# Kernel optimization log

Measured on AMD Instinct MI355X. Metric: run time of the kernel, lower is better.

## Reference

```python
import jax, jax.numpy as jnp
import numpy as np
import math

VOCAB = 50000; D = 512; DEPTH = 6; N = 16; DCONV = 4; R = 32; DFF = 4 * D
B = 2; L = 1024

# A = -exp(A_log) with A_log = log(arange(1..N)) repeated over D  =>  A[d,n] = -(n+1)
A_CONT = -jnp.broadcast_to(jnp.arange(1.0, N + 1, dtype=jnp.float32), (D, N))


def sinusoidal(t, dim):
    half = dim // 2
    f = jnp.exp(jnp.arange(half, dtype=jnp.float32) * (-math.log(10000.0) / (half - 1)))
    e = t.astype(jnp.float32)[:, None] * f[None, :]
    return jnp.concatenate([jnp.sin(e), jnp.cos(e)], axis=-1)


def layernorm(x, g, b, eps=1e-5):
    mu = jnp.mean(x, -1, keepdims=True)
    var = jnp.mean((x - mu) ** 2, -1, keepdims=True)
    return (x - mu) * jax.lax.rsqrt(var + eps) * g + b


def ssm(x, Win, Wconv, Wdt, bdt, Dp, Wout):
    # x: [B,L,D]
    proj = x @ Win.T  # [B,L,2D+R+2N]
    xc, z, dtu, Bp, Cp = jnp.split(proj, [D, 2 * D, 2 * D + R, 2 * D + R + N], axis=-1)
    # depthwise causal conv (left pad d_conv-1 == pad both + truncate to L)
    conv = jax.lax.conv_general_dilated(
        xc.transpose(0, 2, 1), Wconv, (1,), [(DCONV - 1, 0)],
        dimension_numbers=('NCH', 'OIH', 'NCH'), feature_group_count=D)
    u = jax.nn.silu(conv.transpose(0, 2, 1))  # [B,L,D]
    dt = jax.nn.softplus(dtu @ Wdt.T + bdt)   # [B,L,D]
    At = jnp.exp(dt[..., None] * A_CONT)      # [B,L,D,N] (ZOH)
    Bu = ((At - 1.0) / (A_CONT + 1e-10)) * Bp[:, :, None, :] * u[..., None]  # [B,L,D,N]

    def step(h, xs):
        a, bu, c = xs
        h = a * h + bu                       # [B,D,N]
        return h, jnp.einsum('bn,bdn->bd', c, h)

    h0 = jnp.zeros((x.shape[0], D, N), dtype=x.dtype)
    _, ys = jax.lax.scan(step, h0, (At.transpose(1, 0, 2, 3), Bu.transpose(1, 0, 2, 3), Cp.transpose(1, 0, 2)))
    y = ys.transpose(1, 0, 2)                # [B,L,D]
    y = (y + u * Dp) * jax.nn.silu(z)
    return y @ Wout.T


def setup_inputs():
    key = jax.random.key(0)
    ks = iter(jax.random.split(key, 32))
    nrm = lambda shape: jax.random.normal(next(ks), shape, jnp.float32) * 0.02
    inp = {
        'x_t': jax.random.randint(next(ks), (B, L), 0, VOCAB + 1),
        't': jax.random.randint(next(ks), (B,), 0, 100),
        'tok_emb': nrm((VOCAB + 1, D)),
        'tmlp_w1': nrm((4 * D, D)), 'tmlp_b1': jnp.zeros((4 * D,)),
        'tmlp_w2': nrm((D, 4 * D)), 'tmlp_b2': jnp.zeros((D,)),
        'ln1_g': jnp.ones((DEPTH, D)), 'ln1_b': jnp.zeros((DEPTH, D)),
        'in_w': nrm((DEPTH, 2 * D + R + 2 * N, D)),
        'conv_w': nrm((DEPTH, D, 1, DCONV)),
        'dt_w': nrm((DEPTH, D, R)), 'dt_b': jnp.zeros((DEPTH, D)),
        'D_p': jnp.ones((DEPTH, D)),
        'out_w': nrm((DEPTH, D, D)),
        'ln2_g': jnp.ones((DEPTH, D)), 'ln2_b': jnp.zeros((DEPTH, D)),
        'mlp_w1': nrm((DEPTH, DFF, D)), 'mlp_b1': jnp.zeros((DEPTH, DFF)),
        'mlp_w2': nrm((DEPTH, D, DFF)), 'mlp_b2': jnp.zeros((DEPTH, D)),
        'lno_g': jnp.ones((D,)), 'lno_b': jnp.zeros((D,)),
        'head_w': nrm((VOCAB, D)), 'head_b': jnp.zeros((VOCAB,)),
    }
    return inp


def reference(x_t, t, tok_emb, tmlp_w1, tmlp_b1, tmlp_w2, tmlp_b2,
              ln1_g, ln1_b, in_w, conv_w, dt_w, dt_b, D_p, out_w,
              ln2_g, ln2_b, mlp_w1, mlp_b1, mlp_w2, mlp_b2,
              lno_g, lno_b, head_w, head_b):
    te = sinusoidal(t, D)
    te = jax.nn.silu(te @ tmlp_w1.T + tmlp_b1) @ tmlp_w2.T + tmlp_b2  # [B,D]
    x = tok_emb[x_t] + te[:, None, :]                                  # [B,L,D]
    for i in range(DEPTH):
        x = x + ssm(layernorm(x, ln1_g[i], ln1_b[i]),
                    in_w[i], conv_w[i], dt_w[i], dt_b[i], D_p[i], out_w[i])
        h = layernorm(x, ln2_g[i], ln2_b[i])
        x = x + jax.nn.gelu(h @ mlp_w1[i].T + mlp_b1[i], approximate=False) @ mlp_w2[i].T + mlp_b2[i]
    x = layernorm(x, lno_g, lno_b)
    return x @ head_w.T + head_b  # [B,L,VOCAB]
```

## Files before the change

### kernel.cpp

```cpp
#include <hip/hip_runtime.h>
#include <hip/hip_bf16.h>
#include <math.h>

typedef __hip_bfloat16 bf16;
typedef short s16x8 __attribute__((ext_vector_type(8)));
typedef float f32x4 __attribute__((ext_vector_type(4)));

#define M_TOK 2048
#define DD    512
#define LSEQ  1024
#define PW    1088
#define NST   16
#define RR    32
#define DFFW  2048
#define NCH   64
#define CH    16
#define PAD   36
#define NHEAD 50000
#define NHEADP 50048

__device__ __forceinline__ float bf2f(bf16 v) { return __bfloat162float(v); }
__device__ __forceinline__ float siluf(float x) { return x / (1.f + expf(-x)); }

__device__ __forceinline__ s16x8 cvt8(const f32x4& a, const f32x4& b) {
  s16x8 r;
  r[0] = (short)__bfloat16_as_ushort(__float2bfloat16(a[0]));
  r[1] = (short)__bfloat16_as_ushort(__float2bfloat16(a[1]));
  r[2] = (short)__bfloat16_as_ushort(__float2bfloat16(a[2]));
  r[3] = (short)__bfloat16_as_ushort(__float2bfloat16(a[3]));
  r[4] = (short)__bfloat16_as_ushort(__float2bfloat16(b[0]));
  r[5] = (short)__bfloat16_as_ushort(__float2bfloat16(b[1]));
  r[6] = (short)__bfloat16_as_ushort(__float2bfloat16(b[2]));
  r[7] = (short)__bfloat16_as_ushort(__float2bfloat16(b[3]));
  return r;
}

__device__ __forceinline__ void gload16(const bf16* g, bf16* l) {
  __builtin_amdgcn_global_load_lds((const __attribute__((address_space(1))) void*)g,
                                   (__attribute__((address_space(3))) void*)l, 16, 0, 0);
}

__constant__ float c_invn[NST] = {
  -1.f/1, -1.f/2, -1.f/3, -1.f/4, -1.f/5, -1.f/6, -1.f/7, -1.f/8,
  -1.f/9, -1.f/10, -1.f/11, -1.f/12, -1.f/13, -1.f/14, -1.f/15, -1.f/16 };

__global__ __launch_bounds__(256) void k_cvt(
    const float* __restrict__ src, bf16* __restrict__ dst, int n_src, int n_dst)
{
  for (int i = (blockIdx.x * 256 + threadIdx.x) * 8; i < n_dst; i += gridDim.x * 256 * 8) {
    s16x8 v;
    if (i + 8 <= n_src) {
      f32x4 a = *(const f32x4*)(src + i), b = *(const f32x4*)(src + i + 4);
      v = cvt8(a, b);
    } else {
      v = (s16x8){0,0,0,0,0,0,0,0};
    }
    *(s16x8*)((short*)dst + i) = v;
  }
}

__global__ __launch_bounds__(256) void k_te1(
    const int* __restrict__ t, const float* __restrict__ w1, const float* __restrict__ b1,
    float* __restrict__ h1)
{
  __shared__ float semb[2][512];
  int tid = threadIdx.x;
  float t0 = (float)t[0], t1 = (float)t[1];
  {
    int k = tid;
    float f = expf((float)k * (-9.210340371976184f / 255.f));
    semb[0][k]       = sinf(t0 * f);
    semb[0][k + 256] = cosf(t0 * f);
    semb[1][k]       = sinf(t1 * f);
    semb[1][k + 256] = cosf(t1 * f);
  }
  __syncthreads();
  int wave = tid >> 6, lane = tid & 63;
  int j = blockIdx.x * 4 + wave;
  const float* wr = w1 + (size_t)j * 512;
  float s0 = 0.f, s1 = 0.f;
#pragma unroll
  for (int i = 0; i < 8; ++i) {
    int k = lane + (i << 6);
    float wv = wr[k];
    s0 += wv * semb[0][k];
    s1 += wv * semb[1][k];
  }
  for (int o = 32; o; o >>= 1) { s0 += __shfl_down(s0, o); s1 += __shfl_down(s1, o); }
  if (!lane) {
    float bv = b1[j];
    h1[j]        = siluf(s0 + bv);
    h1[2048 + j] = siluf(s1 + bv);
  }
}

__global__ __launch_bounds__(256) void k_te2(
    const float* __restrict__ h1, const float* __restrict__ w2, const float* __restrict__ b2,
    float* __restrict__ te)
{
  __shared__ float sh1[2][2048];
  int tid = threadIdx.x;
  for (int idx = tid; idx < 4096; idx += 256)
    sh1[idx >> 11][idx & 2047] = h1[idx];
  __syncthreads();
  int wave = tid >> 6, lane = tid & 63;
  int d = blockIdx.x * 4 + wave;
  const float* wr = w2 + (size_t)d * 2048;
  float s0 = 0.f, s1 = 0.f;
#pragma unroll
  for (int i = 0; i < 32; ++i) {
    int k = lane + (i << 6);
    float wv = wr[k];
    s0 += wv * sh1[0][k];
    s1 += wv * sh1[1][k];
  }
  for (int o = 32; o; o >>= 1) { s0 += __shfl_down(s0, o); s1 += __shfl_down(s1, o); }
  if (!lane) {
    float bv = b2[d];
    te[d]       = s0 + bv;
    te[512 + d] = s1 + bv;
  }
}

__global__ __launch_bounds__(256) void k_embed(
    const int* __restrict__ x_t, const float* __restrict__ tok,
    const float* __restrict__ te, float* __restrict__ x)
{
  int m = blockIdx.x;
  int b = m >> 10;
  int row = x_t[m];
  const float* src = tok + (size_t)row * DD;
  for (int d = threadIdx.x; d < DD; d += 256)
    x[(size_t)m * DD + d] = src[d] + te[b * DD + d];
}

__global__ __launch_bounds__(256) void k_layernorm(
    const float* __restrict__ x, const float* __restrict__ g, const float* __restrict__ bb,
    bf16* __restrict__ out)
{
  int m = blockIdx.x;
  const float* xr = x + (size_t)m * DD;
  float2 v = ((const float2*)xr)[threadIdx.x];
  float s = v.x + v.y, ss = v.x * v.x + v.y * v.y;
  for (int o = 32; o; o >>= 1) { s += __shfl_down(s, o); ss += __shfl_down(ss, o); }
  __shared__ float ps[4], pss[4];
  int wave = threadIdx.x >> 6, lane = threadIdx.x & 63;
  if (!lane) { ps[wave] = s; pss[wave] = ss; }
  __syncthreads();
  s = ps[0] + ps[1] + ps[2] + ps[3];
  ss = pss[0] + pss[1] + pss[2] + pss[3];
  float mu = s * (1.f / DD);
  float var = ss * (1.f / DD) - mu * mu;
  float inv = rsqrtf(var + 1e-5f);
  int d = threadIdx.x * 2;
  out[(size_t)m * DD + d]     = __float2bfloat16((v.x - mu) * inv * g[d]     + bb[d]);
  out[(size_t)m * DD + d + 1] = __float2bfloat16((v.y - mu) * inv * g[d + 1] + bb[d + 1]);
}

__global__ __launch_bounds__(128) void k_scan1f(
    const float* __restrict__ proj, const float* __restrict__ convw,
    const float* __restrict__ dtw, const float* __restrict__ dtb,
    float* __restrict__ ubuf, float* __restrict__ yloc,
    float* __restrict__ Ebuf, float* __restrict__ Aprod, float* __restrict__ hend)
{
  int d = (blockIdx.x << 7) + threadIdx.x;
  int c = blockIdx.y, b = blockIdx.z;
  int m0 = b * LSEQ + c * CH;
  __shared__ float sBC[CH][32];
  __shared__ float sDT[CH][32];
  for (int idx = threadIdx.x; idx < CH * 32; idx += 128) {
    int l = idx >> 5, j = idx & 31;
    sBC[l][j] = proj[(size_t)(m0 + l) * PW + 2 * DD + RR + j];
    sDT[l][j] = proj[(size_t)(m0 + l) * PW + 2 * DD + j];
  }
  __syncthreads();
  float cw0 = convw[d * 4], cw1 = convw[d * 4 + 1], cw2 = convw[d * 4 + 2], cw3 = convw[d * 4 + 3];
  float dtbd = dtb[d];
  f32x4 wr[8];
#pragma unroll
  for (int i = 0; i < 8; ++i) wr[i] = *(const f32x4*)(dtw + (size_t)d * RR + i * 4);
  float w0 = 0.f, w1 = 0.f, w2 = 0.f;
  {
    int l0 = c * CH;
    if (l0 >= 3) w0 = proj[(size_t)(m0 - 3) * PW + d];
    if (l0 >= 2) w1 = proj[(size_t)(m0 - 2) * PW + d];
    if (l0 >= 1) w2 = proj[(size_t)(m0 - 1) * PW + d];
  }
  float h[NST];
#pragma unroll
  for (int n = 0; n < NST; ++n) h[n] = 0.f;
  float S = 0.f;
  for (int l = 0; l < CH; ++l) {
    size_t m = (size_t)(m0 + l);
    float xc = proj[m * PW + d];
    float cv = w0 * cw0 + w1 * cw1 + w2 * cw2 + xc * cw3;
    w0 = w1; w1 = w2; w2 = xc;
    float uv = siluf(cv);
    ubuf[m * DD + d] = uv;
    float s = dtbd;
#pragma unroll
    for (int i = 0; i < 8; ++i) {
      f32x4 q = *(const f32x4*)&sDT[l][i * 4];
      s += q[0] * wr[i][0] + q[1] * wr[i][1] + q[2] * wr[i][2] + q[3] * wr[i][3];
    }
    float dtv = (s > 0.f) ? (s + log1pf(expf(-s))) : log1pf(expf(s));
    float e1 = expf(-dtv);
    S += dtv;
    Ebuf[m * DD + d] = expf(-S);
    float p = 1.f, acc = 0.f;
#pragma unroll
    for (int n = 0; n < NST; ++n) {
      p *= e1;
      float bu = (p - 1.f) * c_invn[n] * sBC[l][n] * uv;
      h[n] = p * h[n] + bu;
      acc += sBC[l][16 + n] * h[n];
    }
    yloc[m * DD + d] = acc;
  }
  float Ec = expf(-S);
  float p = 1.f;
  size_t base = ((size_t)(b * NCH + c) * NST) * DD + d;
#pragma unroll
  for (int n = 0; n < NST; ++n) {
    p *= Ec;
    Aprod[base + (size_t)n * DD] = p;
    hend [base + (size_t)n * DD] = h[n];
  }
}

__global__ __launch_bounds__(256) void k_scan2w(
    const float* __restrict__ Aprod, const float* __restrict__ hend, float* __restrict__ h0)
{
  int wave = threadIdx.x >> 6, lane = threadIdx.x & 63;
  int chain = blockIdx.x * 4 + wave;
  int d = chain & 511;
  int n = (chain >> 9) & 15;
  int b = chain >> 13;
  size_t o = ((size_t)((b * NCH + lane) * NST + n)) * DD + d;
  float A = Aprod[o], h = hend[o];
#pragma unroll
  for (int off = 1; off < 64; off <<= 1) {
    float Ap = __shfl_up(A, off);
    float hp = __shfl_up(h, off);
    if (lane >= off) { h = A * hp + h; A = A * Ap; }
  }
  float hprev = __shfl_up(h, 1);
  h0[o] = (lane == 0) ? 0.f : hprev;
}

__global__ __launch_bounds__(128) void k_scan3(
    const float* __restrict__ proj, const float* __restrict__ u,
    const float* __restrict__ yloc, const float* __restrict__ Ebuf,
    const float* __restrict__ h0, const float* __restrict__ Dp, bf16* __restrict__ out)
{
  int d = (blockIdx.x << 7) + threadIdx.x;
  int c = blockIdx.y, b = blockIdx.z;
  int m0 = b * LSEQ + c * CH;
  __shared__ float sC[CH][NST];
  for (int idx = threadIdx.x; idx < CH * NST; idx += 128)
    sC[idx >> 4][idx & 15] = proj[(size_t)(m0 + (idx >> 4)) * PW + 2 * DD + RR + NST + (idx & 15)];
  __syncthreads();
  float hh[NST];
  size_t base = ((size_t)(b * NCH + c) * NST) * DD + d;
#pragma unroll
  for (int n = 0; n < NST; ++n) hh[n] = h0[base + (size_t)n * DD];
  float dpv = Dp[d];
  for (int l = 0; l < CH; ++l) {
    size_t m = (size_t)(m0 + l);
    float E = Ebuf[m * DD + d];
    float p = 1.f, corr = 0.f;
#pragma unroll
    for (int n = 0; n < NST; ++n) {
      p *= E;
      corr += sC[l][n] * p * hh[n];
    }
    float y = yloc[m * DD + d] + corr;
    float z = proj[m * PW + DD + d];
    float v = (y + u[m * DD + d] * dpv) * siluf(z);
    out[m * DD + d] = __float2bfloat16(v);
  }
}

template<int ACT, bool BF16OUT, bool RES, bool BIAS>
__global__ __launch_bounds__(256) void gemm_bb64k(
    const bf16* __restrict__ A, const bf16* __restrict__ B,
    const float* __restrict__ bias, const float* __restrict__ res,
    void* __restrict__ Cout, int N, int K)
{
  __shared__ bf16 sA[2][64 * 32];
  __shared__ bf16 sB[2][64 * 32];
  int flat = blockIdx.y * gridDim.x + blockIdx.x;
  int qq = (gridDim.x * gridDim.y) >> 3;
  int s = (flat & 7) * qq + (flat >> 3);
  int bm = (s % gridDim.x) * 64;
  int bn = (s / gridDim.x) * 64;
  int tid = threadIdx.x;
  int wave = tid >> 6, lane = tid & 63;
  int wm = (wave >> 1) << 5, wn = (wave & 1) << 5;
  int r = lane & 15, q = lane >> 4;
  int srow = (wave << 4) + (lane >> 2);
  int scol = (lane & 3) << 3;
  const bf16* pA = A + (size_t)(bm + srow) * K + scol;
  const bf16* pB = B + (size_t)(bn + srow) * K + scol;
  int lofs = (wave << 4) << 5;

  f32x4 acc[2][2];
#pragma unroll
  for (int i = 0; i < 2; ++i)
#pragma unroll
    for (int j = 0; j < 2; ++j) acc[i][j] = (f32x4){0.f, 0.f, 0.f, 0.f};

  for (int k0 = 0; k0 < K; k0 += 64) {
    gload16(pA,      sA[0] + lofs);
    gload16(pA + 32, sA[1] + lofs);
    gload16(pB,      sB[0] + lofs);
    gload16(pB + 32, sB[1] + lofs);
    pA += 64; pB += 64;
    __syncthreads();
#pragma unroll
    for (int kk = 0; kk < 2; ++kk) {
      s16x8 af[2], bg[2];
#pragma unroll
      for (int i = 0; i < 2; ++i) af[i] = *(s16x8*)&sA[kk][((wm + i * 16 + r) << 5) + (q << 3)];
#pragma unroll
      for (int j = 0; j < 2; ++j) bg[j] = *(s16x8*)&sB[kk][((wn + j * 16 + r) << 5) + (q << 3)];
#pragma unroll
      for (int i = 0; i < 2; ++i)
#pragma unroll
        for (int j = 0; j < 2; ++j)
          acc[i][j] = __builtin_amdgcn_mfma_f32_16x16x32_bf16(af[i], bg[j], acc[i][j], 0, 0, 0);
    }
    __syncthreads();
  }

#pragma unroll
  for (int i = 0; i < 2; ++i)
#pragma unroll
    for (int j = 0; j < 2; ++j) {
      int n = bn + wn + j * 16 + r;
#pragma unroll
      for (int e = 0; e < 4; ++e) {
        int m = bm + wm + i * 16 + (q << 2) + e;
        float v = acc[i][j][e];
        if (BIAS) v += bias[n];
        if (ACT == 1) v = 0.5f * v * (1.f + erff(v * 0.70710678118f));
        if (RES) v += res[(size_t)m * N + n];
        if (BF16OUT) ((bf16*)Cout)[(size_t)m * N + n] = __float2bfloat16(v);
        else         ((float*)Cout)[(size_t)m * N + n] = v;
      }
    }
}

template<int ACT, bool BF16OUT, bool RES, bool BIAS>
__global__ __launch_bounds__(256) void gemm_bb128k(
    const bf16* __restrict__ A, const bf16* __restrict__ B,
    const float* __restrict__ bias, const float* __restrict__ res,
    void* __restrict__ Cout, int N, int K)
{
  __shared__ bf16 sA[2][128 * 32];
  __shared__ bf16 sB[2][128 * 32];
  int flat = blockIdx.y * gridDim.x + blockIdx.x;
  int qq = (gridDim.x * gridDim.y) >> 3;
  int s = (flat & 7) * qq + (flat >> 3);
  int bm = (s % gridDim.x) * 128;
  int bn = (s / gridDim.x) * 128;
  int tid = threadIdx.x;
  int wave = tid >> 6, lane = tid & 63;
  int wm = (wave >> 1) << 6, wn = (wave & 1) << 6;
  int r = lane & 15, q = lane >> 4;
  int srow = (wave << 4) + (lane >> 2);
  int scol = (lane & 3) << 3;
  const bf16* pA = A + (size_t)(bm + srow) * K + scol;
  const bf16* pB = B + (size_t)(bn + srow) * K + scol;
  int lofs = (wave << 4) << 5;

  f32x4 acc[4][4];
#pragma unroll
  for (int i = 0; i < 4; ++i)
#pragma unroll
    for (int j = 0; j < 4; ++j) acc[i][j] = (f32x4){0.f, 0.f, 0.f, 0.f};

  for (int k0 = 0; k0 < K; k0 += 64) {
    gload16(pA,                       sA[0] + lofs);
    gload16(pA + (size_t)64 * K,      sA[0] + lofs + 64 * 32);
    gload16(pA + 32,                  sA[1] + lofs);
    gload16(pA + (size_t)64 * K + 32, sA[1] + lofs + 64 * 32);
    gload16(pB,                       sB[0] + lofs);
    gload16(pB + (size_t)64 * K,      sB[0] + lofs + 64 * 32);
    gload16(pB + 32,                  sB[1] + lofs);
    gload16(pB + (size_t)64 * K + 32, sB[1] + lofs + 64 * 32);
    pA += 64; pB += 64;
    __syncthreads();
#pragma unroll
    for (int kk = 0; kk < 2; ++kk) {
      s16x8 af[4], bg[4];
#pragma unroll
      for (int i = 0; i < 4; ++i) af[i] = *(s16x8*)&sA[kk][((wm + i * 16 + r) << 5) + (q << 3)];
#pragma unroll
      for (int j = 0; j < 4; ++j) bg[j] = *(s16x8*)&sB[kk][((wn + j * 16 + r) << 5) + (q << 3)];
#pragma unroll
      for (int i = 0; i < 4; ++i)
#pragma unroll
        for (int j = 0; j < 4; ++j)
          acc[i][j] = __builtin_amdgcn_mfma_f32_16x16x32_bf16(af[i], bg[j], acc[i][j], 0, 0, 0);
    }
    __syncthreads();
  }

#pragma unroll
  for (int i = 0; i < 4; ++i)
#pragma unroll
    for (int j = 0; j < 4; ++j) {
      int n = bn + wn + j * 16 + r;
      if (n >= N) continue;
#pragma unroll
      for (int e = 0; e < 4; ++e) {
        int m = bm + wm + i * 16 + (q << 2) + e;
        float v = acc[i][j][e];
        if (BIAS) v += bias[n];
        if (ACT == 1) v = 0.5f * v * (1.f + erff(v * 0.70710678118f));
        if (RES) v += res[(size_t)m * N + n];
        if (BF16OUT) ((bf16*)Cout)[(size_t)m * N + n] = __float2bfloat16(v);
        else         ((float*)Cout)[(size_t)m * N + n] = v;
      }
    }
}

template<int ACT, bool BF16OUT, bool RES, bool BIAS, bool SWZ>
__global__ __launch_bounds__(256) void gemm_abt(
    const bf16* __restrict__ A, const float* __restrict__ B,
    const float* __restrict__ bias, const float* __restrict__ res,
    void* __restrict__ Cout, int N, int K)
{
  __shared__ bf16 sA[128][PAD];
  __shared__ bf16 sB[128][PAD];
  int bn, bm;
  if (SWZ) {
    int flat = blockIdx.y * gridDim.x + blockIdx.x;
    int q = (gridDim.x * gridDim.y) >> 3;
    int s = (flat & 7) * q + (flat >> 3);
    bm = (s % gridDim.x) * 128;
    bn = (s / gridDim.x) * 128;
  } else {
    bn = blockIdx.x * 128;
    bm = blockIdx.y * 128;
  }
  int tid = threadIdx.x;
  int wave = tid >> 6, lane = tid & 63;
  int wm = (wave >> 1) << 6, wn = (wave & 1) << 6;
  int r = lane & 15, q = lane >> 4;
  int ldr = tid >> 2;
  int ldc = (tid & 3) << 3;
  f32x4 acc[4][4];
#pragma unroll
  for (int i = 0; i < 4; ++i)
#pragma unroll
    for (int j = 0; j < 4; ++j) acc[i][j] = (f32x4){0.f, 0.f, 0.f, 0.f};
  s16x8 pa[2];
  f32x4 pb[2][2];
#define GLOAD(k0)                                                              \
  {                                                                            \
    _Pragma("unroll")                                                          \
    for (int h = 0; h < 2; ++h) {                                              \
      int row = ldr + (h << 6);                                                \
      pa[h] = *(const s16x8*)(A + (size_t)(bm + row) * K + (k0) + ldc);        \
      int nrow = bn + row;                                                     \
      if (nrow < N) {                                                          \
        const float* src = B + (size_t)nrow * K + (k0) + ldc;                  \
        pb[h][0] = *(const f32x4*)src;                                         \
        pb[h][1] = *(const f32x4*)(src + 4);                                   \
      } else {                                                                 \
        pb[h][0] = (f32x4){0.f,0.f,0.f,0.f};                                   \
        pb[h][1] = (f32x4){0.f,0.f,0.f,0.f};                                   \
      }                                                                        \
    }                                                                          \
  }
  GLOAD(0);
  for (int k0 = 0; k0 < K; k0 += 32) {
#pragma unroll
    for (int h = 0; h < 2; ++h) {
      int row = ldr + (h << 6);
      *(s16x8*)&sA[row][ldc] = pa[h];
      *(s16x8*)&sB[row][ldc] = cvt8(pb[h][0], pb[h][1]);
    }
    __syncthreads();
    if (k0 + 32 < K) GLOAD(k0 + 32);
    s16x8 af[4], bg[4];
#pragma unroll
    for (int i = 0; i < 4; ++i) af[i] = *(s16x8*)&sA[wm + i * 16 + r][q << 3];
#pragma unroll
    for (int j = 0; j < 4; ++j) bg[j] = *(s16x8*)&sB[wn + j * 16 + r][q << 3];
#pragma unroll
    for (int i = 0; i < 4; ++i)
#pragma unroll
      for (int j = 0; j < 4; ++j)
        acc[i][j] = __builtin_amdgcn_mfma_f32_16x16x32_bf16(af[i], bg[j], acc[i][j], 0, 0, 0);
    __syncthreads();
  }
#undef GLOAD
#pragma unroll
  for (int i = 0; i < 4; ++i)
#pragma unroll
    for (int j = 0; j < 4; ++j) {
      int n = bn + wn + j * 16 + r;
      if (n >= N) continue;
#pragma unroll
      for (int e = 0; e < 4; ++e) {
        int m = bm + wm + i * 16 + (q << 2) + e;
        float v = acc[i][j][e];
        if (BIAS) v += bias[n];
        if (ACT == 1) v = 0.5f * v * (1.f + erff(v * 0.70710678118f));
        if (RES) v += res[(size_t)m * N + n];
        if (BF16OUT) ((bf16*)Cout)[(size_t)m * N + n] = __float2bfloat16(v);
        else         ((float*)Cout)[(size_t)m * N + n] = v;
      }
    }
}

template<int ACT, bool BF16OUT, bool RES, bool BIAS>
__global__ __launch_bounds__(256) void gemm64(
    const bf16* __restrict__ A, const float* __restrict__ B,
    const float* __restrict__ bias, const float* __restrict__ res,
    void* __restrict__ Cout, int N, int K)
{
  __shared__ bf16 sA[64][PAD];
  __shared__ bf16 sB[64][PAD];
  int bn = blockIdx.x * 64;
  int bm = blockIdx.y * 64;
  int tid = threadIdx.x;
  int wave = tid >> 6, lane = tid & 63;
  int wm = (wave >> 1) << 5, wn = (wave & 1) << 5;
  int r = lane & 15, q = lane >> 4;
  int ldr = tid >> 2;
  int ldc = (tid & 3) << 3;
  f32x4 acc[2][2];
#pragma unroll
  for (int i = 0; i < 2; ++i)
#pragma unroll
    for (int j = 0; j < 2; ++j) acc[i][j] = (f32x4){0.f, 0.f, 0.f, 0.f};
  s16x8 pa;
  f32x4 pb[2];
#define GLOAD64(k0)                                                            \
  {                                                                            \
    pa = *(const s16x8*)(A + (size_t)(bm + ldr) * K + (k0) + ldc);             \
    const float* src = B + (size_t)(bn + ldr) * K + (k0) + ldc;                \
    pb[0] = *(const f32x4*)src;                                                \
    pb[1] = *(const f32x4*)(src + 4);                                          \
  }
  GLOAD64(0);
  for (int k0 = 0; k0 < K; k0 += 32) {
    *(s16x8*)&sA[ldr][ldc] = pa;
    *(s16x8*)&sB[ldr][ldc] = cvt8(pb[0], pb[1]);
    __syncthreads();
    if (k0 + 32 < K) GLOAD64(k0 + 32);
    s16x8 af[2], bg[2];
#pragma unroll
    for (int i = 0; i < 2; ++i) af[i] = *(s16x8*)&sA[wm + i * 16 + r][q << 3];
#pragma unroll
    for (int j = 0; j < 2; ++j) bg[j] = *(s16x8*)&sB[wn + j * 16 + r][q << 3];
#pragma unroll
    for (int i = 0; i < 2; ++i)
#pragma unroll
      for (int j = 0; j < 2; ++j)
        acc[i][j] = __builtin_amdgcn_mfma_f32_16x16x32_bf16(af[i], bg[j], acc[i][j], 0, 0, 0);
    __syncthreads();
  }
#undef GLOAD64
#pragma unroll
  for (int i = 0; i < 2; ++i)
#pragma unroll
    for (int j = 0; j < 2; ++j) {
      int n = bn + wn + j * 16 + r;
#pragma unroll
      for (int e = 0; e < 4; ++e) {
        int m = bm + wm + i * 16 + (q << 2) + e;
        float v = acc[i][j][e];
        if (BIAS) v += bias[n];
        if (ACT == 1) v = 0.5f * v * (1.f + erff(v * 0.70710678118f));
        if (RES) v += res[(size_t)m * N + n];
        if (BF16OUT) ((bf16*)Cout)[(size_t)m * N + n] = __float2bfloat16(v);
        else         ((float*)Cout)[(size_t)m * N + n] = v;
      }
    }
}

extern "C" void kernel_launch(void* const* d_in, const int* in_sizes, int n_in,
                              void* d_out, int out_size, void* d_ws, size_t ws_size,
                              hipStream_t stream) {
  const int*   x_t     = (const int*)d_in[0];
  const int*   t       = (const int*)d_in[1];
  const float* tok_emb = (const float*)d_in[2];
  const float* tmlp_w1 = (const float*)d_in[3];
  const float* tmlp_b1 = (const float*)d_in[4];
  const float* tmlp_w2 = (const float*)d_in[5];
  const float* tmlp_b2 = (const float*)d_in[6];
  const float* ln1_g   = (const float*)d_in[7];
  const float* ln1_b   = (const float*)d_in[8];
  const float* in_w    = (const float*)d_in[9];
  const float* conv_w  = (const float*)d_in[10];
  const float* dt_w    = (const float*)d_in[11];
  const float* dt_b    = (const float*)d_in[12];
  const float* D_p     = (const float*)d_in[13];
  const float* out_w   = (const float*)d_in[14];
  const float* ln2_g   = (const float*)d_in[15];
  const float* ln2_b   = (const float*)d_in[16];
  const float* mlp_w1  = (const float*)d_in[17];
  const float* mlp_b1  = (const float*)d_in[18];
  const float* mlp_w2  = (const float*)d_in[19];
  const float* mlp_b2  = (const float*)d_in[20];
  const float* lno_g   = (const float*)d_in[21];
  const float* lno_b   = (const float*)d_in[22];
  const float* head_w  = (const float*)d_in[23];
  const float* head_b  = (const float*)d_in[24];

  char* w = (char*)d_ws;
  float* te    = (float*)w;  w += 4096;
  float* h1t   = (float*)w;  w += 16384;
  float* x     = (float*)w;  w += (size_t)M_TOK * DD * 4;
  bf16*  aIn   = (bf16*)w;   w += (size_t)M_TOK * DD * 2;
  float* proj  = (float*)w;  w += (size_t)M_TOK * PW * 4;
  float* ubuf  = (float*)w;  w += (size_t)M_TOK * DD * 4;
  float* ybuf  = (float*)w;  w += (size_t)M_TOK * DD * 4;
  float* Ebuf  = (float*)w;  w += (size_t)M_TOK * DD * 4;
  float* Aprod = (float*)w;  w += (size_t)2 * NCH * NST * DD * 4;
  float* hend  = (float*)w;  w += (size_t)2 * NCH * NST * DD * 4;
  float* h0    = (float*)w;  w += (size_t)2 * NCH * NST * DD * 4;
  bf16*  gbuf  = (bf16*)proj;
  bf16* bw_in   = (bf16*)w;  w += (size_t)6 * PW * DD * 2;
  bf16* bw_out  = (bf16*)w;  w += (size_t)6 * DD * DD * 2;
  bf16* bw_m1   = (bf16*)w;  w += (size_t)6 * DFFW * DD * 2;
  bf16* bw_m2   = (bf16*)w;  w += (size_t)6 * DD * DFFW * 2;
  bf16* bw_head = (bf16*)w;  w += (size_t)NHEADP * DD * 2;
  bool fast = ((size_t)(w - (char*)d_ws) <= ws_size);

  if (fast) {
    k_cvt<<<1024, 256, 0, stream>>>(in_w,   bw_in,   6 * PW * DD,   6 * PW * DD);
    k_cvt<<<1024, 256, 0, stream>>>(out_w,  bw_out,  6 * DD * DD,   6 * DD * DD);
    k_cvt<<<1024, 256, 0, stream>>>(mlp_w1, bw_m1,   6 * DFFW * DD, 6 * DFFW * DD);
    k_cvt<<<1024, 256, 0, stream>>>(mlp_w2, bw_m2,   6 * DD * DFFW, 6 * DD * DFFW);
    k_cvt<<<2048, 256, 0, stream>>>(head_w, bw_head, NHEAD * DD,    NHEADP * DD);
  }

  k_te1<<<512, 256, 0, stream>>>(t, tmlp_w1, tmlp_b1, h1t);
  k_te2<<<128, 256, 0, stream>>>(h1t, tmlp_w2, tmlp_b2, te);
  k_embed<<<M_TOK, 256, 0, stream>>>(x_t, tok_emb, te, x);

  for (int i = 0; i < 6; ++i) {
    const float* cw_i   = conv_w + (size_t)i * DD * 4;
    const float* dtw_i  = dt_w   + (size_t)i * DD * RR;
    const float* dtb_i  = dt_b   + (size_t)i * DD;
    const float* dp_i   = D_p    + (size_t)i * DD;
    const float* m1b_i  = mlp_b1 + (size_t)i * DFFW;
    const float* m2b_i  = mlp_b2 + (size_t)i * DD;

    k_layernorm<<<M_TOK, 256, 0, stream>>>(x, ln1_g + i * DD, ln1_b + i * DD, aIn);
    if (fast)
      gemm_bb64k<0,false,false,false><<<dim3(M_TOK / 64, PW / 64), 256, 0, stream>>>(
          aIn, bw_in + (size_t)i * PW * DD, nullptr, nullptr, proj, PW, DD);
    else
      gemm64<0,false,false,false><<<dim3(PW / 64, M_TOK / 64), 256, 0, stream>>>(
          aIn, in_w + (size_t)i * PW * DD, nullptr, nullptr, proj, PW, DD);
    k_scan1f<<<dim3(4, NCH, 2), 128, 0, stream>>>(proj, cw_i, dtw_i, dtb_i,
                                                  ubuf, ybuf, Ebuf, Aprod, hend);
    k_scan2w<<<2 * NST * DD / 4, 256, 0, stream>>>(Aprod, hend, h0);
    k_scan3<<<dim3(4, NCH, 2), 128, 0, stream>>>(proj, ubuf, ybuf, Ebuf, h0, dp_i, aIn);
    if (fast) {
      gemm_bb64k<0,false,true,false><<<dim3(M_TOK / 64, DD / 64), 256, 0, stream>>>(
          aIn, bw_out + (size_t)i * DD * DD, nullptr, x, x, DD, DD);
      k_layernorm<<<M_TOK, 256, 0, stream>>>(x, ln2_g + i * DD, ln2_b + i * DD, aIn);
      gemm_bb64k<1,true,false,true><<<dim3(M_TOK / 64, DFFW / 64), 256, 0, stream>>>(
          aIn, bw_m1 + (size_t)i * DFFW * DD, m1b_i, nullptr, gbuf, DFFW, DD);
      gemm_bb64k<0,false,true,true><<<dim3(M_TOK / 64, DD / 64), 256, 0, stream>>>(
          gbuf, bw_m2 + (size_t)i * DD * DFFW, m2b_i, x, x, DD, DFFW);
    } else {
      gemm64<0,false,true,false><<<dim3(DD / 64, M_TOK / 64), 256, 0, stream>>>(
          aIn, out_w + (size_t)i * DD * DD, nullptr, x, x, DD, DD);
      k_layernorm<<<M_TOK, 256, 0, stream>>>(x, ln2_g + i * DD, ln2_b + i * DD, aIn);
      gemm64<1,true,false,true><<<dim3(DFFW / 64, M_TOK / 64), 256, 0, stream>>>(
          aIn, mlp_w1 + (size_t)i * DFFW * DD, m1b_i, nullptr, gbuf, DFFW, DD);
      gemm64<0,false,true,true><<<dim3(DD / 64, M_TOK / 64), 256, 0, stream>>>(
          gbuf, mlp_w2 + (size_t)i * DD * DFFW, m2b_i, x, x, DD, DFFW);
    }
  }

  k_layernorm<<<M_TOK, 256, 0, stream>>>(x, lno_g, lno_b, aIn);
  if (fast)
    gemm_bb128k<0,false,false,true><<<dim3(M_TOK / 128, NHEADP / 128), 256, 0, stream>>>(
        aIn, bw_head, head_b, nullptr, d_out, NHEAD, DD);
  else
    gemm_abt<0,false,false,true,true><<<dim3(M_TOK / 128, (NHEAD + 127) / 128), 256, 0, stream>>>(
        aIn, head_w, head_b, nullptr, d_out, NHEAD, DD);
}
```

Baseline: 1.086 ms.

## Use 256x256 double-buffered tile GEMM for vocab head projection

Replaces the 128x128 head GEMM with a dedicated 512-thread kernel using 256x256 output tiles, so each wave computes a 128x64 sub-tile. It also adds prefetch double-buffering over K=32 slices, loading the next slice while MFMAs run on the current one. The padded head width is raised to a multiple of 256 so the grid tiles evenly. The aim is more operand reuse per LDS byte and hiding global load latency, at the cost of higher register pressure (128 accumulator floats per thread) and more padded work at the vocab edge.

```diff
diff --git a/kernel.cpp b/kernel.cpp
--- a/kernel.cpp
+++ b/kernel.cpp
@@ -17,7 +17,7 @@
 #define CH    16
 #define PAD   36
 #define NHEAD 50000
-#define NHEADP 50048
+#define NHEADP 50176
 
 __device__ __forceinline__ float bf2f(bf16 v) { return __bfloat162float(v); }
 __device__ __forceinline__ float siluf(float x) { return x / (1.f + expf(-x)); }
@@ -351,22 +351,22 @@
     }
 }
 
-template<int ACT, bool BF16OUT, bool RES, bool BIAS>
-__global__ __launch_bounds__(256) void gemm_bb128k(
+template<bool BIAS>
+__global__ __launch_bounds__(512) void gemm_bhead256(
     const bf16* __restrict__ A, const bf16* __restrict__ B,
-    const float* __restrict__ bias, const float* __restrict__ res,
-    void* __restrict__ Cout, int N, int K)
-{
-  __shared__ bf16 sA[2][128 * 32];
-  __shared__ bf16 sB[2][128 * 32];
+    const float* __restrict__ bias, float* __restrict__ C, int N, int K)
+{
+  __shared__ bf16 sA[2][256 * 32];
+  __shared__ bf16 sB[2][256 * 32];
   int flat = blockIdx.y * gridDim.x + blockIdx.x;
   int qq = (gridDim.x * gridDim.y) >> 3;
   int s = (flat & 7) * qq + (flat >> 3);
-  int bm = (s % gridDim.x) * 128;
-  int bn = (s / gridDim.x) * 128;
+  int bm = (s % gridDim.x) * 256;
+  int bn = (s / gridDim.x) * 256;
   int tid = threadIdx.x;
   int wave = tid >> 6, lane = tid & 63;
-  int wm = (wave >> 1) << 6, wn = (wave & 1) << 6;
+  int wm = (wave >> 2) << 7;
+  int wn = (wave & 3) << 6;
   int r = lane & 15, q = lane >> 4;
   int srow = (wave << 4) + (lane >> 2);
   int scol = (lane & 3) << 3;
@@ -374,41 +374,44 @@
   const bf16* pB = B + (size_t)(bn + srow) * K + scol;
   int lofs = (wave << 4) << 5;
 
-  f32x4 acc[4][4];
-#pragma unroll
-  for (int i = 0; i < 4; ++i)
+  f32x4 acc[8][4];
+#pragma unroll
+  for (int i = 0; i < 8; ++i)
 #pragma unroll
     for (int j = 0; j < 4; ++j) acc[i][j] = (f32x4){0.f, 0.f, 0.f, 0.f};
 
-  for (int k0 = 0; k0 < K; k0 += 64) {
-    gload16(pA,                       sA[0] + lofs);
-    gload16(pA + (size_t)64 * K,      sA[0] + lofs + 64 * 32);
-    gload16(pA + 32,                  sA[1] + lofs);
-    gload16(pA + (size_t)64 * K + 32, sA[1] + lofs + 64 * 32);
-    gload16(pB,                       sB[0] + lofs);
-    gload16(pB + (size_t)64 * K,      sB[0] + lofs + 64 * 32);
-    gload16(pB + 32,                  sB[1] + lofs);
-    gload16(pB + (size_t)64 * K + 32, sB[1] + lofs + 64 * 32);
-    pA += 64; pB += 64;
+  gload16(pA,                   sA[0] + lofs);
+  gload16(pA + (size_t)128 * K, sA[0] + lofs + 128 * 32);
+  gload16(pB,                   sB[0] + lofs);
+  gload16(pB + (size_t)128 * K, sB[0] + lofs + 128 * 32);
+  pA += 32; pB += 32;
+  __syncthreads();
+
+  int cur = 0;
+  for (int k0 = 0; k0 < K; k0 += 32) {
+    if (k0 + 32 < K) {
+      gload16(pA,                   sA[cur ^ 1] + lofs);
+      gload16(pA + (size_t)128 * K, sA[cur ^ 1] + lofs + 128 * 32);
+      gload16(pB,                   sB[cur ^ 1] + lofs);
+      gload16(pB + (size_t)128 * K, sB[cur ^ 1] + lofs + 128 * 32);
+      pA += 32; pB += 32;
+    }
+    s16x8 bg[4];
+#pragma unroll
+    for (int j = 0; j < 4; ++j) bg[j] = *(s16x8*)&sB[cur][((wn + j * 16 + r) << 5) + (q << 3)];
+#pragma unroll
+    for (int i = 0; i < 8; ++i) {
+      s16x8 af = *(s16x8*)&sA[cur][((wm + i * 16 + r) << 5) + (q << 3)];
+#pragma unroll
+      for (int j = 0; j < 4; ++j)
+        acc[i][j] = __builtin_amdgcn_mfma_f32_16x16x32_bf16(af, bg[j], acc[i][j], 0, 0, 0);
+    }
     __syncthreads();
-#pragma unroll
-    for (int kk = 0; kk < 2; ++kk) {
-      s16x8 af[4], bg[4];
-#pragma unroll
-      for (int i = 0; i < 4; ++i) af[i] = *(s16x8*)&sA[kk][((wm + i * 16 + r) << 5) + (q << 3)];
-#pragma unroll
-      for (int j = 0; j < 4; ++j) bg[j] = *(s16x8*)&sB[kk][((wn + j * 16 + r) << 5) + (q << 3)];
-#pragma unroll
-      for (int i = 0; i < 4; ++i)
-#pragma unroll
-        for (int j = 0; j < 4; ++j)
-          acc[i][j] = __builtin_amdgcn_mfma_f32_16x16x32_bf16(af[i], bg[j], acc[i][j], 0, 0, 0);
-    }
-    __syncthreads();
-  }
-
-#pragma unroll
-  for (int i = 0; i < 4; ++i)
+    cur ^= 1;
+  }
+
+#pragma unroll
+  for (int i = 0; i < 8; ++i)
 #pragma unroll
     for (int j = 0; j < 4; ++j) {
       int n = bn + wn + j * 16 + r;
@@ -418,10 +421,7 @@
         int m = bm + wm + i * 16 + (q << 2) + e;
         float v = acc[i][j][e];
         if (BIAS) v += bias[n];
-        if (ACT == 1) v = 0.5f * v * (1.f + erff(v * 0.70710678118f));
-        if (RES) v += res[(size_t)m * N + n];
-        if (BF16OUT) ((bf16*)Cout)[(size_t)m * N + n] = __float2bfloat16(v);
-        else         ((float*)Cout)[(size_t)m * N + n] = v;
+        C[(size_t)m * N + n] = v;
       }
     }
 }
@@ -685,8 +685,8 @@
 
   k_layernorm<<<M_TOK, 256, 0, stream>>>(x, lno_g, lno_b, aIn);
   if (fast)
-    gemm_bb128k<0,false,false,true><<<dim3(M_TOK / 128, NHEADP / 128), 256, 0, stream>>>(
-        aIn, bw_head, head_b, nullptr, d_out, NHEAD, DD);
+    gemm_bhead256<true><<<dim3(M_TOK / 256, NHEADP / 256), 512, 0, stream>>>(
+        aIn, bw_head, head_b, (float*)d_out, NHEAD, DD);
   else
     gemm_abt<0,false,false,true,true><<<dim3(M_TOK / 128, (NHEAD + 127) / 128), 256, 0, stream>>>(
         aIn, head_w, head_b, nullptr, d_out, NHEAD, DD);
```

New measurement: 1.113 ms. +2.5%, slower.
